# Performance work log

Measured on AMD Instinct MI355X. Metric: run time of the kernel, lower is better.

Reference implementation:

```python
import jax, jax.numpy as jnp
import numpy as np

_N = 2048          # matrix_size (A_sparse.shape[0] in the original)
_NNZ = 32768       # number of factor / pred entries
_LOGCOND_EPS = 1e-12


def setup_inputs() -> dict:
    key = jax.random.key(0)
    k1, k2, k3, k4, k5 = jax.random.split(key, 5)
    pred_values = jax.random.normal(k1, (_NNZ,), dtype=jnp.float32)
    active_scales = jax.random.uniform(k2, (_NNZ,), dtype=jnp.float32) * 0.05
    A_factor = jax.random.normal(k3, (_N, _N), dtype=jnp.float32)
    factor_rows = jax.random.randint(k4, (_NNZ,), 0, _N, dtype=jnp.int32)
    factor_cols = jax.random.randint(k5, (_NNZ,), 0, _N, dtype=jnp.int32)
    return {
        "pred_values": pred_values,
        "active_scales": active_scales,
        "A_factor": A_factor,
        "factor_rows": factor_rows,
        "factor_cols": factor_cols,
    }


def reference(pred_values, active_scales, A_factor, factor_rows, factor_cols):
    n = A_factor.shape[0]
    dt = pred_values.dtype
    # SPD system matrix A (stands in for the original fixed A_sparse)
    A = A_factor @ A_factor.T / jnp.asarray(n, dt) + jnp.eye(n, dtype=dt)
    # Sparse factor L assembled from predicted values (scatter-add, dup-safe),
    # unit diagonal keeps L A L^T well conditioned / SPD.
    L = jnp.eye(n, dtype=dt).at[factor_rows, factor_cols].add(pred_values * active_scales)
    # Preconditioned matrix M = L A L^T (symmetric PSD)
    M = L @ A @ L.T
    M = 0.5 * (M + M.T)
    evals = jnp.linalg.eigvalsh(M)  # ascending
    lam_min = jnp.maximum(evals[0], _LOGCOND_EPS)
    lam_max = jnp.maximum(evals[-1], _LOGCOND_EPS)
    # loss = log(lambda_max) - log(lambda_min) = log condition number
    return jnp.log(lam_max) - jnp.log(lam_min)
```

## Files before the change

### kernel.cpp

```cpp
#include <hip/hip_runtime.h>

#define N2 2048
#define NNZ 32768
#define LK 22
#define NBL 128
#define BINCAP 64

typedef __attribute__((ext_vector_type(8))) _Float16 half8;
typedef __attribute__((ext_vector_type(4))) float f32x4;

#define AGENT __HIP_MEMORY_SCOPE_AGENT
#define AS1C(p) ((const __attribute__((address_space(1))) unsigned int*)(p))
#define AS3(p)  ((__attribute__((address_space(3))) unsigned int*)(p))

__device__ __forceinline__ unsigned short f2h(float f) {
  _Float16 h = (_Float16)f;
  return *(unsigned short*)&h;
}


__global__ __launch_bounds__(256) void convert_kernel(const float* __restrict__ W,
                                                      unsigned short* __restrict__ Hf,
                                                      unsigned* __restrict__ cntR,
                                                      unsigned* __restrict__ cntC) {
  if (blockIdx.x < 8)       cntR[blockIdx.x * 256 + threadIdx.x] = 0;
  else if (blockIdx.x < 16) cntC[(blockIdx.x - 8) * 256 + threadIdx.x] = 0;
  int i4 = blockIdx.x * 256 + threadIdx.x;
  float4 w = ((const float4*)W)[i4];
  ushort4 h;
  h.x = f2h(w.x); h.y = f2h(w.y); h.z = f2h(w.z); h.w = f2h(w.w);
  ((ushort4*)Hf)[i4] = h;
}

__global__ __launch_bounds__(256) void fill_kernel(const float* __restrict__ pred,
                                                   const float* __restrict__ scal,
                                                   const int* __restrict__ rows,
                                                   const int* __restrict__ cols,
                                                   unsigned* __restrict__ cntR,
                                                   int* __restrict__ binRc,
                                                   float* __restrict__ binRv,
                                                   unsigned* __restrict__ cntC,
                                                   int* __restrict__ binCr,
                                                   float* __restrict__ binCv) {
  int k = blockIdx.x * 256 + threadIdx.x;
  int r = rows[k], c = cols[k];
  float v = pred[k] * scal[k];
  unsigned pR = atomicAdd(&cntR[r], 1u);
  if (pR < BINCAP) { binRc[r * BINCAP + pR] = c; binRv[r * BINCAP + pR] = v; }
  unsigned pC = atomicAdd(&cntC[c], 1u);
  if (pC < BINCAP) { binCr[c * BINCAP + pC] = r; binCv[c * BINCAP + pC] = v; }
}

__global__ __launch_bounds__(256) void gatherG_kernel(const unsigned* __restrict__ cntR,
                                                      const int* __restrict__ binRc,
                                                      const float* __restrict__ binRv,
                                                      const unsigned short* __restrict__ Hf,
                                                      unsigned short* __restrict__ Gh) {
  const int r = blockIdx.x, tid = threadIdx.x;
  __shared__ int scol_[BINCAP];
  __shared__ float sval_[BINCAP];
  const unsigned ne = min(cntR[r], (unsigned)BINCAP);
  if (tid < ne) {
    scol_[tid] = binRc[r * BINCAP + tid];
    sval_[tid] = binRv[r * BINCAP + tid];
  }
  __syncthreads();
  uint4 own = *(const uint4*)(Hf + (size_t)r * 2048 + tid * 8);
  half8 ho = *(half8*)&own;
  float acc[8];
#pragma unroll
  for (int k = 0; k < 8; ++k) acc[k] = (float)ho[k];
  unsigned e = 0;
  for (; e + 8 <= ne; e += 8) {
    uint4 q[8];
#pragma unroll
    for (int u = 0; u < 8; ++u)
      q[u] = *(const uint4*)(Hf + (size_t)scol_[e + u] * 2048 + tid * 8);
#pragma unroll
    for (int u = 0; u < 8; ++u) {
      half8 hv = *(half8*)&q[u];
      const float v = sval_[e + u];
#pragma unroll
      for (int k = 0; k < 8; ++k) acc[k] += v * (float)hv[k];
    }
  }
  for (; e + 4 <= ne; e += 4) {
    uint4 q[4];
#pragma unroll
    for (int u = 0; u < 4; ++u)
      q[u] = *(const uint4*)(Hf + (size_t)scol_[e + u] * 2048 + tid * 8);
#pragma unroll
    for (int u = 0; u < 4; ++u) {
      half8 hv = *(half8*)&q[u];
      const float v = sval_[e + u];
#pragma unroll
      for (int k = 0; k < 8; ++k) acc[k] += v * (float)hv[k];
    }
  }
  for (; e < ne; ++e) {
    uint4 qq = *(const uint4*)(Hf + (size_t)scol_[e] * 2048 + tid * 8);
    half8 hv = *(half8*)&qq;
    const float v = sval_[e];
#pragma unroll
    for (int k = 0; k < 8; ++k) acc[k] += v * (float)hv[k];
  }
  unsigned short o[8];
#pragma unroll
  for (int k = 0; k < 8; ++k) o[k] = f2h(acc[k]);
  *(uint4*)(Gh + (size_t)r * 2048 + tid * 8) = *(uint4*)o;
}

__device__ __forceinline__ void stage_tiles2(const unsigned short* __restrict__ X,
                                             unsigned short* Xb, unsigned short* Yb,
                                             int row0, int col0, int kk,
                                             int srowX, int srowY, int scol, int wq) {
  __builtin_amdgcn_global_load_lds(
      AS1C(X + (size_t)(row0 + srowX) * 2048 + kk + scol),
      AS3(Xb + (wq * 16) * 32), 16, 0, 0);
#pragma unroll
  for (int q = 0; q < 2; ++q) {
    __builtin_amdgcn_global_load_lds(
        AS1C(X + (size_t)(col0 + srowY + q * 16) * 2048 + kk + scol),
        AS3(Yb + (wq * 32 + q * 16) * 32), 16, 0, 0);
  }
}

__global__ __launch_bounds__(512) void gemmM_kernel(const unsigned short* __restrict__ Gh,
                                                    float* __restrict__ M) {
  const int tid = threadIdx.x;
  int bi, bj;
  bool diag;
  if (blockIdx.x < 32) {
    bi = blockIdx.x; bj = bi >> 1; diag = true;
  } else {
    int idx = blockIdx.x - 32;
    int j = 0;
    while (j < 14 && idx >= (j + 1) * (30 - j)) ++j;
    bj = j;
    bi = 2 * j + 2 + (idx - j * (31 - j));
    diag = false;
  }

  __shared__ __align__(16) char smem[49152];
  unsigned short* Xs = (unsigned short*)smem;
  unsigned short* Ys = (unsigned short*)(smem + 16384);
  float* Cred = (float*)smem;

  const int w = tid >> 6, lane = tid & 63;
  const int half = w >> 2, wq = w & 3;
  const int row0 = bi * 64, col0 = bj * 128;
  const int m0 = (wq & 1) * 32, n0 = (wq >> 1) * 64;
  f32x4 acc[2][4];
#pragma unroll
  for (int a = 0; a < 2; ++a)
#pragma unroll
    for (int b = 0; b < 4; ++b) acc[a][b] = (f32x4){0.f, 0.f, 0.f, 0.f};
  const int mrow = lane & 15, kseg = (lane >> 4) * 8;
  const int srowX = wq * 16 + (lane >> 2);
  const int srowY = wq * 32 + (lane >> 2);
  const int scol = (lane & 3) * 8;
  const int kbase = half * 1024;

  stage_tiles2(Gh, Xs + (half * 2 + 0) * 2048, Ys + (half * 2 + 0) * 4096,
               row0, col0, kbase, srowX, srowY, scol, wq);
  for (int t = 0; t < 32; ++t) {
    const int cur = t & 1;
    __syncthreads();
    if (t < 31)
      stage_tiles2(Gh, Xs + (half * 2 + (cur ^ 1)) * 2048,
                   Ys + (half * 2 + (cur ^ 1)) * 4096,
                   row0, col0, kbase + (t + 1) * 32, srowX, srowY, scol, wq);
    const unsigned short* Xb = Xs + (half * 2 + cur) * 2048;
    const unsigned short* Yb = Ys + (half * 2 + cur) * 4096;
    half8 af[2], bf[4];
#pragma unroll
    for (int q = 0; q < 2; ++q)
      af[q] = *(const half8*)(Xb + (m0 + q * 16 + mrow) * 32 + kseg);
#pragma unroll
    for (int q = 0; q < 4; ++q)
      bf[q] = *(const half8*)(Yb + (n0 + q * 16 + mrow) * 32 + kseg);
#pragma unroll
    for (int mt = 0; mt < 2; ++mt)
#pragma unroll
      for (int nt = 0; nt < 4; ++nt)
        acc[mt][nt] = __builtin_amdgcn_mfma_f32_16x16x32_f16(af[mt], bf[nt], acc[mt][nt], 0, 0, 0);
  }
  const int crow = (lane >> 4) * 4, ccol = lane & 15;
  __syncthreads();
  if (half == 1) {
#pragma unroll
    for (int mt = 0; mt < 2; ++mt)
#pragma unroll
      for (int nt = 0; nt < 4; ++nt)
#pragma unroll
        for (int r = 0; r < 4; ++r)
          Cred[(m0 + mt * 16 + crow + r) * 132 + n0 + nt * 16 + ccol] = acc[mt][nt][r];
  }
  __syncthreads();
  if (half == 0) {
    const float invn = 1.0f / 2048.0f;
#pragma unroll
    for (int mt = 0; mt < 2; ++mt)
#pragma unroll
      for (int nt = 0; nt < 4; ++nt) {
        const int gi0 = row0 + m0 + mt * 16 + crow;
        const int gj = col0 + n0 + nt * 16 + ccol;
        size_t base = (size_t)gi0 * 2048 + gj;
#pragma unroll
        for (int r = 0; r < 4; ++r) {
          const int li = (m0 + mt * 16 + crow + r) * 132 + n0 + nt * 16 + ccol;
          float val = (acc[mt][nt][r] + Cred[li]) * invn +
                      ((gi0 + r == gj) ? 1.0f : 0.0f);
          M[base + (size_t)r * 2048] = val;
          if (!diag) Cred[li] = val;
        }
      }
  }
  if (!diag) {
    __syncthreads();
    const int orow = tid >> 2;
    const int cseg = (tid & 3) * 16;
    float mv[16];
#pragma unroll
    for (int k = 0; k < 16; ++k)
      mv[k] = Cred[(cseg + k) * 132 + orow];
    float4* dst = (float4*)(M + (size_t)(col0 + orow) * 2048 + row0 + cseg);
    dst[0] = (float4){mv[0], mv[1], mv[2], mv[3]};
    dst[1] = (float4){mv[4], mv[5], mv[6], mv[7]};
    dst[2] = (float4){mv[8], mv[9], mv[10], mv[11]};
    dst[3] = (float4){mv[12], mv[13], mv[14], mv[15]};
  }
}

__device__ __forceinline__ float block_sum8(float v, float* red) {
#pragma unroll
  for (int off = 32; off; off >>= 1) v += __shfl_down(v, off);
  if ((threadIdx.x & 63) == 0) red[threadIdx.x >> 6] = v;
  __syncthreads();
  float r = ((red[0] + red[1]) + (red[2] + red[3])) +
            ((red[4] + red[5]) + (red[6] + red[7]));
  __syncthreads();
  return r;
}

__global__ __launch_bounds__(512) void lanczos_kernel(const float* __restrict__ M,
                                                      const unsigned* __restrict__ cntR,
                                                      const int* __restrict__ binRc,
                                                      const float* __restrict__ binRv,
                                                      const unsigned* __restrict__ cntC,
                                                      const int* __restrict__ binCr,
                                                      const float* __restrict__ binCv,
                                                      unsigned long long* __restrict__ Z0,
                                                      unsigned long long* __restrict__ Z1,
                                                      float* __restrict__ out) {
  const int tid = threadIdx.x, b = blockIdx.x;
  const int wave = tid >> 6, lane = tid & 63;
  __shared__ __align__(16) float Mlds[16 * 2048];
  __shared__ __align__(16) float VA[2048];
  __shared__ __align__(16) float VB[2048];
  __shared__ float red[8];
  __shared__ float al[LK + 2], b2[LK + 2];
  __shared__ float bnds[2], res[2];

  const float* Mblk = M + (size_t)b * 16 * 2048;
#pragma unroll
  for (int q = 0; q < 16; ++q)
    __builtin_amdgcn_global_load_lds(AS1C(Mblk + wave * 4096 + q * 256 + lane * 4),
                                     AS3(Mlds + wave * 4096 + q * 256), 16, 0, 0);

  float pv[4];
  float part = 0.f;
#pragma unroll
  for (int t = 0; t < 4; ++t) {
    int i = t * 512 + tid;
    unsigned u = (unsigned)i * 2654435761u;
    u ^= u >> 16; u *= 2246822519u; u ^= u >> 13;
    float rv = (float)(u >> 8) * (2.f / 16777216.f) - 1.f;
    pv[t] = rv;
    part += rv * rv;
  }
  float nrm = block_sum8(part, red);
  float innm = rsqrtf(nrm);
#pragma unroll
  for (int t = 0; t < 4; ++t) {
    int i = t * 512 + tid;
    VA[i] = pv[t] * innm;
    VB[i] = 0.f;
  }
  __syncthreads();

  for (int rr = 0; rr < 2; ++rr) {
    const int r = b * 16 + wave * 2 + rr;
    float* Mrow = Mlds + (wave * 2 + rr) * 2048;
    const unsigned nR = min(cntR[r], (unsigned)BINCAP);
    const unsigned nC = min(cntC[r], (unsigned)BINCAP);
    int c_ = 0; float v_ = 0.f; unsigned n_ = 0;
    if (lane < nR) {
      c_ = binRc[r * BINCAP + lane];
      v_ = binRv[r * BINCAP + lane];
      n_ = min(cntC[c_], (unsigned)BINCAP);
    }
    if (lane < nR) atomicAdd(&Mrow[c_], v_);
    if (lane < nC)
      atomicAdd(&Mrow[binCr[r * BINCAP + lane]], binCv[r * BINCAP + lane]);
    const unsigned g = lane >> 4, p0 = lane & 15;
    for (unsigned e = g; e < nR; e += 4) {
      const int c = __shfl(c_, (int)e);
      const float v = __shfl(v_, (int)e);
      const unsigned n2 = __shfl(n_, (int)e);
      for (unsigned p = p0; p < n2; p += 16)
        atomicAdd(&Mrow[binCr[c * BINCAP + p]], v * binCv[c * BINCAP + p]);
    }
  }
  __syncthreads();

  float* Vcur = VA;
  float* Vprev = VB;
  float beta_prev = 0.f;

  for (int j = 1; j <= LK; ++j) {
    unsigned long long* Z = (j & 1) ? Z0 : Z1;
#pragma unroll
    for (int rr = 0; rr < 2; ++rr) {
      const int r = b * 16 + wave * 2 + rr;
      const float4* Mr = (const float4*)(Mlds + (wave * 2 + rr) * 2048);
      float s = 0.f;
#pragma unroll
      for (int t = 0; t < 8; ++t) {
        int idx = t * 64 + lane;
        float4 m4 = Mr[idx];
        float4 v4 = ((const float4*)Vcur)[idx];
        s += m4.x * v4.x + m4.y * v4.y + m4.z * v4.z + m4.w * v4.w;
      }
#pragma unroll
      for (int off = 32; off; off >>= 1) s += __shfl_down(s, off);
      if (lane == 0) {
        float zv = s - beta_prev * Vprev[r];
        unsigned long long pk = ((unsigned long long)(unsigned)j << 32) |
                                (unsigned long long)(unsigned)__float_as_uint(zv);
        __hip_atomic_store(&Z[r], pk, __ATOMIC_RELAXED, AGENT);
      }
    }

    float va[4];
#pragma unroll
    for (int t = 0; t < 4; ++t) va[t] = Vcur[t * 512 + tid];

    unsigned long long w4[4];
    int rounds = 0;
    for (;;) {
      bool ok = true;
#pragma unroll
      for (int t = 0; t < 4; ++t) {
        w4[t] = __hip_atomic_load(&Z[t * 512 + tid], __ATOMIC_RELAXED, AGENT);
        ok &= ((unsigned)(w4[t] >> 32) == (unsigned)j);
      }
      if (ok) break;
      if (rounds == 1)      __builtin_amdgcn_s_sleep(1);
      else if (rounds == 2) __builtin_amdgcn_s_sleep(2);
      else if (rounds >= 3) __builtin_amdgcn_s_sleep(8);
      ++rounds;
    }
    float za[4];
    float pa = 0.f;
#pragma unroll
    for (int t = 0; t < 4; ++t) {
      za[t] = __uint_as_float((unsigned)w4[t]);
      pa += za[t] * va[t];
    }
    float alpha = block_sum8(pa, red);
    float pb = 0.f;
#pragma unroll
    for (int t = 0; t < 4; ++t) {
      float rsd = za[t] - alpha * va[t];
      pb += rsd * rsd;
    }
    float beta2 = block_sum8(pb, red);
    float beta = sqrtf(fmaxf(beta2, 1e-30f));
    float invb = 1.f / beta;
    if (tid == 0) { al[j] = alpha; b2[j] = beta2; }
#pragma unroll
    for (int t = 0; t < 4; ++t) {
      int i = t * 512 + tid;
      Vprev[i] = (za[t] - alpha * va[t]) * invb;
    }
    float* tmp = Vprev; Vprev = Vcur; Vcur = tmp;
    beta_prev = beta;
    __syncthreads();
  }

  if (b == 0) {
    if (tid == 0) {
      float lo = 1e30f, hi = -1e30f;
      for (int i = 1; i <= LK; ++i) {
        float bl = (i > 1) ? sqrtf(b2[i - 1]) : 0.f;
        float br = (i < LK) ? sqrtf(b2[i]) : 0.f;
        lo = fminf(lo, al[i] - bl - br);
        hi = fmaxf(hi, al[i] + bl + br);
      }
      bnds[0] = lo; bnds[1] = hi;
    }
    __syncthreads();
    if (wave < 2) {
      const int tcount = (wave == 0) ? 1 : LK;
      float lo = bnds[0], hi = bnds[1];
      for (int round = 0; round < 4; ++round) {
        float x = lo + (hi - lo) * (float)(lane + 1) * (1.f / 65.f);
        int cnt = 0;
        float d = al[1] - x;
        if (fabsf(d) < 1e-25f) d = -1e-25f;
        if (d < 0.f) cnt++;
        for (int i = 2; i <= LK; ++i) {
          d = (al[i] - x) - b2[i - 1] / d;
          if (fabsf(d) < 1e-25f) d = -1e-25f;
          if (d < 0.f) cnt++;
        }
        bool ab = (cnt >= tcount);
        float cand_hi = ab ? x : hi;
        float cand_lo = ab ? lo : x;
#pragma unroll
        for (int off = 32; off; off >>= 1) {
          cand_hi = fminf(cand_hi, __shfl_down(cand_hi, off));
          cand_lo = fmaxf(cand_lo, __shfl_down(cand_lo, off));
        }
        cand_hi = __shfl(cand_hi, 0);
        cand_lo = __shfl(cand_lo, 0);
        hi = cand_hi;
        lo = fminf(cand_lo, hi);
      }
      if (lane == 0) res[wave] = 0.5f * (lo + hi);
    }
    __syncthreads();
    if (tid == 0) {
      float lmin = fmaxf(res[0], 1e-12f);
      float lmax = fmaxf(res[1], 1e-12f);
      out[0] = logf(lmax) - logf(lmin);
    }
  }
}

extern "C" void kernel_launch(void* const* d_in, const int* in_sizes, int n_in,
                              void* d_out, int out_size, void* d_ws, size_t ws_size,
                              hipStream_t stream) {
  const float* pred = (const float*)d_in[0];
  const float* scal = (const float*)d_in[1];
  const float* W    = (const float*)d_in[2];
  const int*   rows = (const int*)d_in[3];
  const int*   cols = (const int*)d_in[4];
  float* out = (float*)d_out;

  char* ws = (char*)d_ws;
  const size_t MB = 1024 * 1024;
  unsigned short* Hf = (unsigned short*)(ws);
  unsigned short* Gh = (unsigned short*)(ws + 8 * MB);
  float* M = (float*)(ws + 16 * MB);
  char* ctrl = ws + 32 * MB;
  unsigned* cntR = (unsigned*)(ctrl);
  unsigned* cntC = (unsigned*)(ctrl + 8192);
  int*      binRc = (int*)(ctrl + 16384);
  float*    binRv = (float*)(ctrl + 16384 + 524288);
  int*      binCr = (int*)(ctrl + 16384 + 2 * 524288);
  float*    binCv = (float*)(ctrl + 16384 + 3 * 524288);
  unsigned long long* Z0 = (unsigned long long*)(ctrl + 16384 + 4 * 524288);
  unsigned long long* Z1 = (unsigned long long*)(ctrl + 16384 + 4 * 524288 + 16384);

  convert_kernel<<<4096, 256, 0, stream>>>(W, Hf, cntR, cntC);
  fill_kernel<<<NNZ / 256, 256, 0, stream>>>(pred, scal, rows, cols,
                                             cntR, binRc, binRv, cntC, binCr, binCv);
  gatherG_kernel<<<2048, 256, 0, stream>>>(cntR, binRc, binRv, Hf, Gh);
  gemmM_kernel<<<272, 512, 0, stream>>>(Gh, M);
  lanczos_kernel<<<NBL, 512, 0, stream>>>(M, cntR, binRc, binRv,
                                          cntC, binCr, binCv, Z0, Z1, out);
}
```

Before: 246.7 us.

## Retile symmetric GEMM to 128x128 blocks with XOR-swizzled LDS staging

The symmetric M = G G^T kernel moves from 64x128 tiles with a two-way split-K reduction to full 128x128 tiles over the upper triangle, halving the block count from 272 to 136. Each of 8 waves now owns 16 rows across all 128 columns, and LDS staging uses 64-wide K steps with an XOR swizzle to avoid bank conflicts. This removes the split-K LDS reduction and raises data reuse per tile. The trade-off is fewer blocks than CUs, which may underfill the device, and the transposed write-back now runs as per-wave rounds with narrower stores.

```diff
diff --git a/kernel.cpp b/kernel.cpp
--- a/kernel.cpp
+++ b/kernel.cpp
@@ -110,18 +110,20 @@
   *(uint4*)(Gh + (size_t)r * 2048 + tid * 8) = *(uint4*)o;
 }
 
-__device__ __forceinline__ void stage_tiles2(const unsigned short* __restrict__ X,
-                                             unsigned short* Xb, unsigned short* Yb,
-                                             int row0, int col0, int kk,
-                                             int srowX, int srowY, int scol, int wq) {
-  __builtin_amdgcn_global_load_lds(
-      AS1C(X + (size_t)(row0 + srowX) * 2048 + kk + scol),
-      AS3(Xb + (wq * 16) * 32), 16, 0, 0);
+__device__ __forceinline__ void stageXY(const unsigned short* __restrict__ Gh,
+                                        char* Xb, char* Yb,
+                                        int row0, int col0, int k0,
+                                        int w, int lane) {
+  const int srcc = ((lane & 7) * 16) ^ ((lane >> 3) << 4);
 #pragma unroll
   for (int q = 0; q < 2; ++q) {
+    const int rl = w * 16 + q * 8 + (lane >> 3);
     __builtin_amdgcn_global_load_lds(
-        AS1C(X + (size_t)(col0 + srowY + q * 16) * 2048 + kk + scol),
-        AS3(Yb + (wq * 32 + q * 16) * 32), 16, 0, 0);
+        AS1C((const char*)(Gh + (size_t)(row0 + rl) * 2048 + k0) + srcc),
+        AS3(Xb + (w * 16 + q * 8) * 128), 16, 0, 0);
+    __builtin_amdgcn_global_load_lds(
+        AS1C((const char*)(Gh + (size_t)(col0 + rl) * 2048 + k0) + srcc),
+        AS3(Yb + (w * 16 + q * 8) * 128), 16, 0, 0);
   }
 }
 
@@ -130,105 +132,87 @@
   const int tid = threadIdx.x;
   int bi, bj;
   bool diag;
-  if (blockIdx.x < 32) {
-    bi = blockIdx.x; bj = bi >> 1; diag = true;
+  if (blockIdx.x < 16) {
+    bi = bj = blockIdx.x; diag = true;
   } else {
-    int idx = blockIdx.x - 32;
+    int idx = blockIdx.x - 16;
     int j = 0;
-    while (j < 14 && idx >= (j + 1) * (30 - j)) ++j;
+    while (j < 15) {
+      int offn = 15 * (j + 1) - (j + 1) * j / 2;
+      if (idx < offn) break;
+      ++j;
+    }
     bj = j;
-    bi = 2 * j + 2 + (idx - j * (31 - j));
+    int off = 15 * j - j * (j - 1) / 2;
+    bi = j + 1 + (idx - off);
     diag = false;
   }
 
-  __shared__ __align__(16) char smem[49152];
-  unsigned short* Xs = (unsigned short*)smem;
-  unsigned short* Ys = (unsigned short*)(smem + 16384);
-  float* Cred = (float*)smem;
+  __shared__ __align__(16) char smem[65536];
+  float* LDSf = (float*)smem;
 
   const int w = tid >> 6, lane = tid & 63;
-  const int half = w >> 2, wq = w & 3;
-  const int row0 = bi * 64, col0 = bj * 128;
-  const int m0 = (wq & 1) * 32, n0 = (wq >> 1) * 64;
-  f32x4 acc[2][4];
-#pragma unroll
-  for (int a = 0; a < 2; ++a)
-#pragma unroll
-    for (int b = 0; b < 4; ++b) acc[a][b] = (f32x4){0.f, 0.f, 0.f, 0.f};
-  const int mrow = lane & 15, kseg = (lane >> 4) * 8;
-  const int srowX = wq * 16 + (lane >> 2);
-  const int srowY = wq * 32 + (lane >> 2);
-  const int scol = (lane & 3) * 8;
-  const int kbase = half * 1024;
-
-  stage_tiles2(Gh, Xs + (half * 2 + 0) * 2048, Ys + (half * 2 + 0) * 4096,
-               row0, col0, kbase, srowX, srowY, scol, wq);
+  const int row0 = bi * 128, col0 = bj * 128;
+  const int mrow = lane & 15;
+  const int crow = (lane >> 4) * 4, ccol = lane & 15;
+  f32x4 acc[8];
+#pragma unroll
+  for (int n = 0; n < 8; ++n) acc[n] = (f32x4){0.f, 0.f, 0.f, 0.f};
+
+  stageXY(Gh, smem, smem + 32768, row0, col0, 0, w, lane);
+
+  const int arow = w * 16 + mrow;
+  const int xswA = (mrow & 7) << 4;
   for (int t = 0; t < 32; ++t) {
-    const int cur = t & 1;
     __syncthreads();
     if (t < 31)
-      stage_tiles2(Gh, Xs + (half * 2 + (cur ^ 1)) * 2048,
-                   Ys + (half * 2 + (cur ^ 1)) * 4096,
-                   row0, col0, kbase + (t + 1) * 32, srowX, srowY, scol, wq);
-    const unsigned short* Xb = Xs + (half * 2 + cur) * 2048;
-    const unsigned short* Yb = Ys + (half * 2 + cur) * 4096;
-    half8 af[2], bf[4];
-#pragma unroll
-    for (int q = 0; q < 2; ++q)
-      af[q] = *(const half8*)(Xb + (m0 + q * 16 + mrow) * 32 + kseg);
-#pragma unroll
-    for (int q = 0; q < 4; ++q)
-      bf[q] = *(const half8*)(Yb + (n0 + q * 16 + mrow) * 32 + kseg);
-#pragma unroll
-    for (int mt = 0; mt < 2; ++mt)
-#pragma unroll
-      for (int nt = 0; nt < 4; ++nt)
-        acc[mt][nt] = __builtin_amdgcn_mfma_f32_16x16x32_f16(af[mt], bf[nt], acc[mt][nt], 0, 0, 0);
-  }
-  const int crow = (lane >> 4) * 4, ccol = lane & 15;
-  __syncthreads();
-  if (half == 1) {
-#pragma unroll
-    for (int mt = 0; mt < 2; ++mt)
-#pragma unroll
-      for (int nt = 0; nt < 4; ++nt)
-#pragma unroll
-        for (int r = 0; r < 4; ++r)
-          Cred[(m0 + mt * 16 + crow + r) * 132 + n0 + nt * 16 + ccol] = acc[mt][nt][r];
-  }
-  __syncthreads();
-  if (half == 0) {
-    const float invn = 1.0f / 2048.0f;
-#pragma unroll
-    for (int mt = 0; mt < 2; ++mt)
-#pragma unroll
-      for (int nt = 0; nt < 4; ++nt) {
-        const int gi0 = row0 + m0 + mt * 16 + crow;
-        const int gj = col0 + n0 + nt * 16 + ccol;
-        size_t base = (size_t)gi0 * 2048 + gj;
-#pragma unroll
-        for (int r = 0; r < 4; ++r) {
-          const int li = (m0 + mt * 16 + crow + r) * 132 + n0 + nt * 16 + ccol;
-          float val = (acc[mt][nt][r] + Cred[li]) * invn +
-                      ((gi0 + r == gj) ? 1.0f : 0.0f);
-          M[base + (size_t)r * 2048] = val;
-          if (!diag) Cred[li] = val;
-        }
-      }
+      stageXY(Gh, smem + ((t + 1) & 1) * 16384, smem + 32768 + ((t + 1) & 1) * 16384,
+              row0, col0, (t + 1) * 64, w, lane);
+    const char* Xb = smem + (t & 1) * 16384;
+    const char* Yb = smem + 32768 + (t & 1) * 16384;
+#pragma unroll
+    for (int kk = 0; kk < 2; ++kk) {
+      const int cb = kk * 64 + (lane >> 4) * 16;
+      half8 af = *(const half8*)(Xb + arow * 128 + (cb ^ xswA));
+#pragma unroll
+      for (int nt = 0; nt < 8; ++nt) {
+        const int nrow = nt * 16 + mrow;
+        half8 bf = *(const half8*)(Yb + nrow * 128 + (cb ^ ((nrow & 7) << 4)));
+        acc[nt] = __builtin_amdgcn_mfma_f32_16x16x32_f16(af, bf, acc[nt], 0, 0, 0);
+      }
+    }
+  }
+  const float invn = 1.0f / 2048.0f;
+  float vals[8][4];
+#pragma unroll
+  for (int nt = 0; nt < 8; ++nt) {
+    const int gj = col0 + nt * 16 + ccol;
+#pragma unroll
+    for (int r = 0; r < 4; ++r) {
+      const int gi = row0 + w * 16 + crow + r;
+      float v = acc[nt][r] * invn + ((gi == gj) ? 1.0f : 0.0f);
+      vals[nt][r] = v;
+      M[(size_t)gi * 2048 + gj] = v;
+    }
   }
   if (!diag) {
     __syncthreads();
-    const int orow = tid >> 2;
-    const int cseg = (tid & 3) * 16;
-    float mv[16];
-#pragma unroll
-    for (int k = 0; k < 16; ++k)
-      mv[k] = Cred[(cseg + k) * 132 + orow];
-    float4* dst = (float4*)(M + (size_t)(col0 + orow) * 2048 + row0 + cseg);
-    dst[0] = (float4){mv[0], mv[1], mv[2], mv[3]};
-    dst[1] = (float4){mv[4], mv[5], mv[6], mv[7]};
-    dst[2] = (float4){mv[8], mv[9], mv[10], mv[11]};
-    dst[3] = (float4){mv[12], mv[13], mv[14], mv[15]};
+    for (int round = 0; round < 2; ++round) {
+      if ((w >> 2) == round) {
+        float* myc = LDSf + (w & 3) * (16 * 132);
+#pragma unroll
+        for (int nt = 0; nt < 8; ++nt)
+#pragma unroll
+          for (int r = 0; r < 4; ++r)
+            myc[(crow + r) * 132 + nt * 16 + ccol] = vals[nt][r];
+        for (int u = 0; u < 32; ++u) {
+          const int jj = u * 4 + (lane >> 4);
+          const int ii = lane & 15;
+          M[(size_t)(col0 + jj) * 2048 + row0 + w * 16 + ii] = myc[ii * 132 + jj];
+        }
+      }
+      __syncthreads();
+    }
   }
 }
 
@@ -468,7 +452,7 @@
   fill_kernel<<<NNZ / 256, 256, 0, stream>>>(pred, scal, rows, cols,
                                              cntR, binRc, binRv, cntC, binCr, binCv);
   gatherG_kernel<<<2048, 256, 0, stream>>>(cntR, binRc, binRv, Hf, Gh);
-  gemmM_kernel<<<272, 512, 0, stream>>>(Gh, M);
+  gemmM_kernel<<<136, 512, 0, stream>>>(Gh, M);
   lanczos_kernel<<<NBL, 512, 0, stream>>>(M, cntR, binRc, binRv,
                                           cntC, binCr, binCv, Z0, Z1, out);
 }
```

Measured after the change: 245.4 us, median of 2. Within noise of the previous version (-0.5%).
